# Kernel tuning notes

Measured on AMD Instinct MI355X. Metric: run time of the kernel, lower is better.

The kernel has to match this reference:

```python
import jax, jax.numpy as jnp
import numpy as np

D_MODEL = 1024
N_HEADS = 16
D_HEAD = D_MODEL // N_HEADS


def setup_inputs() -> dict:
    key = jax.random.key(0)
    ks = jax.random.split(key, 9)
    s = 1.0 / np.sqrt(D_MODEL)
    return {
        "x": jax.random.normal(ks[0], (4, 2048, D_MODEL), dtype=jnp.float32),
        "w_q": jax.random.uniform(ks[1], (D_MODEL, D_MODEL), jnp.float32, -s, s),
        "b_q": jax.random.uniform(ks[2], (D_MODEL,), jnp.float32, -s, s),
        "w_k": jax.random.uniform(ks[3], (D_MODEL, D_MODEL), jnp.float32, -s, s),
        "b_k": jax.random.uniform(ks[4], (D_MODEL,), jnp.float32, -s, s),
        "w_v": jax.random.uniform(ks[5], (D_MODEL, D_MODEL), jnp.float32, -s, s),
        "b_v": jax.random.uniform(ks[6], (D_MODEL,), jnp.float32, -s, s),
        "w_o": jax.random.uniform(ks[7], (D_MODEL, D_MODEL), jnp.float32, -s, s),
        "b_o": jax.random.uniform(ks[8], (D_MODEL,), jnp.float32, -s, s),
    }


def reference(x, w_q, b_q, w_k, b_k, w_v, b_v, w_o, b_o):
    B, S, _ = x.shape
    # Projections (torch Linear: x @ W.T + b), split into heads -> [B, H, S, Dh]
    def proj(w, b):
        return (x @ w.T + b).reshape(B, S, N_HEADS, D_HEAD).transpose(0, 2, 1, 3)

    q = proj(w_q, b_q)
    k = proj(w_k, b_k)
    v = proj(w_v, b_v)

    scale = 1.0 / np.sqrt(D_HEAD).astype(np.float32)
    scores = jnp.einsum("bhqd,bhkd->bhqk", q, k) * scale  # [B,H,S,S]
    attn = jax.nn.softmax(scores, axis=-1)  # dropout is identity in eval mode
    ctx = jnp.einsum("bhqk,bhkd->bhqd", attn, v)  # [B,H,S,Dh]
    ctx = ctx.transpose(0, 2, 1, 3).reshape(B, S, D_MODEL)
    return ctx @ w_o.T + b_o
```

## Files before the change

kernel.cpp:

```cpp
#include <hip/hip_runtime.h>
#include <hip/hip_bf16.h>

#define B_  4
#define S_  2048
#define D_  1024
#define H_  16
#define DH  64
#define M_  (B_ * S_)

typedef unsigned short u16;
typedef unsigned int u32;
typedef __attribute__((ext_vector_type(8))) short bf16x8;
typedef __attribute__((ext_vector_type(4))) float f32x4;
typedef __attribute__((ext_vector_type(4))) unsigned short u16x4;
typedef __attribute__((ext_vector_type(4))) unsigned int u32x4;

static __device__ __forceinline__ u16 f2bf(float x) {
    union { float f; unsigned u; } c;
    c.f = x;
    const unsigned u = c.u;
    return (u16)((u + 0x7FFFu + ((u >> 16) & 1u)) >> 16);
}
static __device__ __forceinline__ float bf2f(u16 h) {
    union { unsigned u; float f; } c;
    c.u = ((unsigned)h) << 16;
    return c.f;
}
#ifdef __BF16_MANT_DIG__
static __device__ __forceinline__ u16 f2bf_hw(float x) {
    __bf16 b = (__bf16)x;
    return __builtin_bit_cast(u16, b);
}
#else
#define f2bf_hw f2bf
#endif
#if __has_builtin(__builtin_amdgcn_exp2f)
#define fexp2 __builtin_amdgcn_exp2f
#else
#define fexp2 exp2f
#endif
static __device__ __forceinline__ void gl16(const u16* g, u16* l) {
    __builtin_amdgcn_global_load_lds(
        (const __attribute__((address_space(1))) unsigned int*)g,
        (__attribute__((address_space(3))) unsigned int*)l, 16, 0, 0);
}
static __device__ __forceinline__ u32 cvtpk(float a, float b) {
    u32 r;
    asm("v_cvt_pk_bf16_f32 %0, %1, %2" : "=v"(r) : "v"(a), "v"(b));
    return r;
}
static __device__ __forceinline__ void pswap32(u32& d, u32& s) {
    asm volatile("v_permlane32_swap_b32 %0, %1" : "+v"(d), "+v"(s));
}
static __device__ __forceinline__ void pswap16(u32& d, u32& s) {
    asm volatile("v_permlane16_swap_b32 %0, %1" : "+v"(d), "+v"(s));
}

__global__ __launch_bounds__(256) void prep(const float* __restrict__ x,
                                            const float* __restrict__ wq,
                                            const float* __restrict__ wk,
                                            const float* __restrict__ wv,
                                            const float* __restrict__ wo,
                                            u16* __restrict__ xh,
                                            u16* __restrict__ wh,
                                            u16* __restrict__ woh,
                                            u16* __restrict__ wol) {
    const size_t NX = (size_t)M_ * D_ / 4;
    const size_t NW = (size_t)D_ * D_ / 4;
    const size_t i = (size_t)blockIdx.x * 256 + threadIdx.x;
    if (i < NX) {
        float4 v = ((const float4*)x)[i];
        u16x4 h;
        h[0] = f2bf_hw(v.x); h[1] = f2bf_hw(v.y);
        h[2] = f2bf_hw(v.z); h[3] = f2bf_hw(v.w);
        ((u16x4*)xh)[i] = h;
    } else if (i < NX + 3 * NW) {
        const size_t j = i - NX;
        const int sel = (int)(j / NW);
        const size_t k = j - (size_t)sel * NW;
        const float* src = sel == 0 ? wq : sel == 1 ? wk : wv;
        float4 v = ((const float4*)src)[k];
        u16x4 h;
        h[0] = f2bf_hw(v.x); h[1] = f2bf_hw(v.y);
        h[2] = f2bf_hw(v.z); h[3] = f2bf_hw(v.w);
        ((u16x4*)(wh + (size_t)sel * D_ * D_))[k] = h;
    } else {
        const size_t k = i - NX - 3 * NW;
        float4 v = ((const float4*)wo)[k];
        u16x4 h, l;
        float vv[4] = {v.x, v.y, v.z, v.w};
#pragma unroll
        for (int j = 0; j < 4; ++j) {
            h[j] = f2bf_hw(vv[j]);
            l[j] = f2bf_hw(vv[j] - bf2f(h[j]));
        }
        ((u16x4*)woh)[k] = h;
        ((u16x4*)wol)[k] = l;
    }
}

__global__ __launch_bounds__(256) void gemm_qkv(const u16* __restrict__ xh,
                                                const u16* __restrict__ whb,
                                                const float* __restrict__ bq,
                                                const float* __restrict__ bk,
                                                const float* __restrict__ bv,
                                                u16* __restrict__ qb,
                                                u16* __restrict__ kb,
                                                u16* __restrict__ vt) {
    __shared__ __align__(16) u16 sA[8192];
    __shared__ __align__(16) u16 sB[8192];

    const int tid = threadIdx.x;
    const int l = tid & 63;
    const int w = tid >> 6;
    const int lo = l & 15;
    const int hi = l >> 4;
    const int wr = w >> 1;
    const int wc = w & 1;
    const int L = blockIdx.x;
    const int c = L & 7;
    const int t = L >> 3;
    const int by = c * 8 + (t & 7);
    const int bxs = t >> 3;
    const int wsel = bxs >> 3;
    const int bx = bxs & 7;
    const int m0 = by * 128;
    const int n0 = bx * 128;

    const u16* W = whb + (size_t)wsel * D_ * D_;
    const float* bias = wsel == 0 ? bq : wsel == 1 ? bk : bv;

    auto stage = [&](int k0, int half) {
#pragma unroll
        for (int i = 0; i < 2; ++i) {
            const int p = 256 * i + tid;
            const int row = p >> 2;
            const int ps = p & 3;
            const int sl = ps ^ ((row + (row >> 2)) & 3);
            const int lb = half * 4096 + (256 * i + 64 * w) * 8;
            gl16(xh + (size_t)(m0 + row) * D_ + k0 + 8 * sl, &sA[lb]);
            gl16(W + (size_t)(n0 + row) * D_ + k0 + 8 * sl, &sB[lb]);
        }
    };

    const f32x4 z4 = {0.f, 0.f, 0.f, 0.f};
    f32x4 acc[4][4];
#pragma unroll
    for (int i = 0; i < 4; ++i)
#pragma unroll
        for (int j = 0; j < 4; ++j) acc[i][j] = z4;

    stage(0, 0);
    for (int k0 = 0; k0 < D_; k0 += 32) {
        const int cur = (k0 >> 5) & 1;
        __syncthreads();
        if (k0 + 32 < D_) stage(k0 + 32, cur ^ 1);
        const int bufo = cur * 4096;

        bf16x8 ah[4], bh[4];
#pragma unroll
        for (int mi = 0; mi < 4; ++mi) {
            const int r = wr * 64 + mi * 16 + lo;
            const int sl = hi ^ ((r + (r >> 2)) & 3);
            ah[mi] = *(const bf16x8*)&sA[bufo + r * 32 + sl * 8];
        }
#pragma unroll
        for (int nj = 0; nj < 4; ++nj) {
            const int r = wc * 64 + nj * 16 + lo;
            const int sl = hi ^ ((r + (r >> 2)) & 3);
            bh[nj] = *(const bf16x8*)&sB[bufo + r * 32 + sl * 8];
        }
#pragma unroll
        for (int mi = 0; mi < 4; ++mi)
#pragma unroll
            for (int nj = 0; nj < 4; ++nj)
                acc[mi][nj] = __builtin_amdgcn_mfma_f32_16x16x32_bf16(
                    ah[mi], bh[nj], acc[mi][nj], 0, 0, 0);
    }

    float bv_[4];
#pragma unroll
    for (int nj = 0; nj < 4; ++nj) bv_[nj] = bias[n0 + wc * 64 + nj * 16 + lo];

#pragma unroll
    for (int mi = 0; mi < 4; ++mi)
#pragma unroll
        for (int nj = 0; nj < 4; ++nj)
#pragma unroll
            for (int r = 0; r < 4; ++r) {
                const float v = acc[mi][nj][r] + bv_[nj];
                const int cm = m0 + wr * 64 + mi * 16 + hi * 4 + r;
                const int cn = n0 + wc * 64 + nj * 16 + lo;
                const int b = cm >> 11, s = cm & (S_ - 1);
                const int h = cn >> 6, d = cn & 63;
                if (wsel == 0)
                    qb[(((size_t)b * H_ + h) * S_ + s) * DH + d] =
                        f2bf(v * 0.18033688011112042f);
                else if (wsel == 1)
                    kb[(((size_t)b * H_ + h) * S_ + s) * DH + d] = f2bf(v);
                else
                    vt[(((size_t)b * H_ + h) * DH + d) * S_ + s] = f2bf(v);
            }
}

__global__ __launch_bounds__(256) void gemm_out(const u16* __restrict__ Ah,
                                                const u16* __restrict__ Al,
                                                const u16* __restrict__ Wh,
                                                const u16* __restrict__ Wl,
                                                const float* __restrict__ bias,
                                                float* __restrict__ Cout) {
    __shared__ __align__(16) u16 sAh[8192];
    __shared__ __align__(16) u16 sBh[8192];
    __shared__ __align__(16) u16 sAl[8192];
    __shared__ __align__(16) u16 sBl[8192];

    const int tid = threadIdx.x;
    const int l = tid & 63;
    const int w = tid >> 6;
    const int lo = l & 15;
    const int hi = l >> 4;
    const int wr = w >> 1;
    const int wc = w & 1;
    const int L = blockIdx.x;
    const int c = L & 7;
    const int t = L >> 3;
    const int by = c * 8 + (t >> 3);
    const int bx = t & 7;
    const int m0 = by * 128;
    const int n0 = bx * 128;

    auto stage = [&](int k0, int half) {
#pragma unroll
        for (int i = 0; i < 2; ++i) {
            const int p = 256 * i + tid;
            const int row = p >> 2;
            const int ps = p & 3;
            const int sl = ps ^ ((row + (row >> 2)) & 3);
            const int lb = half * 4096 + (256 * i + 64 * w) * 8;
            const size_t ga = (size_t)(m0 + row) * D_ + k0 + 8 * sl;
            const size_t gb = (size_t)(n0 + row) * D_ + k0 + 8 * sl;
            gl16(Ah + ga, &sAh[lb]);
            gl16(Al + ga, &sAl[lb]);
            gl16(Wh + gb, &sBh[lb]);
            gl16(Wl + gb, &sBl[lb]);
        }
    };

    const f32x4 z4 = {0.f, 0.f, 0.f, 0.f};
    f32x4 acc[4][4];
#pragma unroll
    for (int i = 0; i < 4; ++i)
#pragma unroll
        for (int j = 0; j < 4; ++j) acc[i][j] = z4;

    stage(0, 0);
    for (int k0 = 0; k0 < D_; k0 += 32) {
        const int cur = (k0 >> 5) & 1;
        __syncthreads();
        if (k0 + 32 < D_) stage(k0 + 32, cur ^ 1);
        const int bufo = cur * 4096;

        bf16x8 ah[4], al_[4], bh[4], bl_[4];
#pragma unroll
        for (int mi = 0; mi < 4; ++mi) {
            const int r = wr * 64 + mi * 16 + lo;
            const int sl = hi ^ ((r + (r >> 2)) & 3);
            ah[mi] = *(const bf16x8*)&sAh[bufo + r * 32 + sl * 8];
            al_[mi] = *(const bf16x8*)&sAl[bufo + r * 32 + sl * 8];
        }
#pragma unroll
        for (int nj = 0; nj < 4; ++nj) {
            const int r = wc * 64 + nj * 16 + lo;
            const int sl = hi ^ ((r + (r >> 2)) & 3);
            bh[nj] = *(const bf16x8*)&sBh[bufo + r * 32 + sl * 8];
            bl_[nj] = *(const bf16x8*)&sBl[bufo + r * 32 + sl * 8];
        }
#pragma unroll
        for (int mi = 0; mi < 4; ++mi)
#pragma unroll
            for (int nj = 0; nj < 4; ++nj) {
                acc[mi][nj] = __builtin_amdgcn_mfma_f32_16x16x32_bf16(
                    ah[mi], bh[nj], acc[mi][nj], 0, 0, 0);
                acc[mi][nj] = __builtin_amdgcn_mfma_f32_16x16x32_bf16(
                    ah[mi], bl_[nj], acc[mi][nj], 0, 0, 0);
                acc[mi][nj] = __builtin_amdgcn_mfma_f32_16x16x32_bf16(
                    al_[mi], bh[nj], acc[mi][nj], 0, 0, 0);
            }
    }

    float bv_[4];
#pragma unroll
    for (int nj = 0; nj < 4; ++nj) bv_[nj] = bias[n0 + wc * 64 + nj * 16 + lo];

#pragma unroll
    for (int mi = 0; mi < 4; ++mi)
#pragma unroll
        for (int nj = 0; nj < 4; ++nj)
#pragma unroll
            for (int r = 0; r < 4; ++r) {
                const int cm = m0 + wr * 64 + mi * 16 + hi * 4 + r;
                const int cn = n0 + wc * 64 + nj * 16 + lo;
                Cout[(size_t)cm * D_ + cn] = acc[mi][nj][r] + bv_[nj];
            }
}

__global__ __launch_bounds__(256, 4) void attn6(const u16* __restrict__ Qb,
                                                const u16* __restrict__ Kb,
                                                const u16* __restrict__ Vtg,
                                                u16* __restrict__ chi,
                                                u16* __restrict__ clo) {
    __shared__ __align__(16) u16 KsA[2 * 4096];
    __shared__ __align__(16) u16 VsA[2 * 4096];

    const int tid = threadIdx.x;
    const int l = tid & 63;
    const int w = tid >> 6;
    const int lo = l & 15;
    const int hi = l >> 4;
    const int L = blockIdx.x;
    const int c = L & 7;
    const int t = L >> 3;
    const int bh = c * 8 + (t >> 4);
    const int s0 = (t & 15) * 128;
    const size_t base = (size_t)bh * S_ * DH;

    const int sp0 = tid;
    const int srow0 = sp0 >> 3, ssl0 = (sp0 & 7) ^ (srow0 & 7);
    const int sp1 = 256 + tid;
    const int srow1 = sp1 >> 3, ssl1 = (sp1 & 7) ^ (srow1 & 7);
    const int lb0 = (64 * w) * 8;
    const int lb1 = (256 + 64 * w) * 8;

    bf16x8 qa[2][2];
#pragma unroll
    for (int qh = 0; qh < 2; ++qh) {
        const u16* qp = Qb + base + (size_t)(s0 + w * 32 + qh * 16 + lo) * DH;
        qa[qh][0] = *(const bf16x8*)(qp + hi * 8);
        qa[qh][1] = *(const bf16x8*)(qp + hi * 8 + 32);
    }

    const f32x4 zero4 = {0.f, 0.f, 0.f, 0.f};
    f32x4 acc[2][4];
    f32x4 acc_l[2] = {zero4, zero4};
#pragma unroll
    for (int qh = 0; qh < 2; ++qh)
#pragma unroll
        for (int g = 0; g < 4; ++g) acc[qh][g] = zero4;

    const short onebf = (short)0x3F80;
    const bf16x8 ones = {onebf, onebf, onebf, onebf, onebf, onebf, onebf, onebf};

#define STAGE(KT, HALF)                                                        \
    do {                                                                       \
        const size_t kbase = base + (size_t)(KT) * 64 * DH;                    \
        const size_t vbase = base + (size_t)(KT) * 64;                         \
        gl16(Kb + kbase + (size_t)srow0 * DH + 8 * ssl0, &KsA[(HALF)*4096 + lb0]); \
        gl16(Vtg + vbase + (size_t)srow0 * S_ + 8 * ssl0, &VsA[(HALF)*4096 + lb0]); \
        gl16(Kb + kbase + (size_t)srow1 * DH + 8 * ssl1, &KsA[(HALF)*4096 + lb1]); \
        gl16(Vtg + vbase + (size_t)srow1 * S_ + 8 * ssl1, &VsA[(HALF)*4096 + lb1]); \
    } while (0)

    STAGE(0, 0);

    for (int kt = 0; kt < S_ / 64; ++kt) {
        const int cur = kt & 1;
        __syncthreads();
        if (kt + 1 < S_ / 64) STAGE(kt + 1, cur ^ 1);
        const u16* Ks = &KsA[cur * 4096];
        const u16* Vs = &VsA[cur * 4096];

        f32x4 sc[2][4];
#pragma unroll
        for (int qh = 0; qh < 2; ++qh)
#pragma unroll
            for (int f = 0; f < 4; ++f) sc[qh][f] = zero4;
        __builtin_amdgcn_s_setprio(1);
#pragma unroll
        for (int f = 0; f < 4; ++f) {
            const int kr = lo + 16 * f;
            const int ksw = (kr & 7) << 3;
#pragma unroll
            for (int ks = 0; ks < 2; ++ks) {
                bf16x8 kf = *(const bf16x8*)&Ks[kr * 64 + ((hi * 8 + 32 * ks) ^ ksw)];
                sc[0][f] = __builtin_amdgcn_mfma_f32_16x16x32_bf16(kf, qa[0][ks], sc[0][f], 0, 0, 0);
                sc[1][f] = __builtin_amdgcn_mfma_f32_16x16x32_bf16(kf, qa[1][ks], sc[1][f], 0, 0, 0);
            }
        }
        __builtin_amdgcn_s_setprio(0);

        bf16x8 pa[2][2];
#pragma unroll
        for (int qh = 0; qh < 2; ++qh) {
            u32 T[2][4];
#pragma unroll
            for (int ks = 0; ks < 2; ++ks)
#pragma unroll
                for (int cc = 0; cc < 2; ++cc) {
                    u32 X = cvtpk(fexp2(sc[qh][2 * ks][2 * cc]),
                                  fexp2(sc[qh][2 * ks][2 * cc + 1]));
                    u32 Y = cvtpk(fexp2(sc[qh][2 * ks + 1][2 * cc]),
                                  fexp2(sc[qh][2 * ks + 1][2 * cc + 1]));
                    pswap32(X, Y);
                    pswap16(X, Y);
                    T[ks][cc] = X;
                    T[ks][2 + cc] = Y;
                }
#pragma unroll
            for (int ks = 0; ks < 2; ++ks) {
                u32x4 word = {T[ks][0], T[ks][1], T[ks][2], T[ks][3]};
                pa[qh][ks] = __builtin_bit_cast(bf16x8, word);
            }
        }

        __builtin_amdgcn_s_setprio(1);
        acc_l[0] = __builtin_amdgcn_mfma_f32_16x16x32_bf16(ones, pa[0][0], acc_l[0], 0, 0, 0);
        acc_l[0] = __builtin_amdgcn_mfma_f32_16x16x32_bf16(ones, pa[0][1], acc_l[0], 0, 0, 0);
        acc_l[1] = __builtin_amdgcn_mfma_f32_16x16x32_bf16(ones, pa[1][0], acc_l[1], 0, 0, 0);
        acc_l[1] = __builtin_amdgcn_mfma_f32_16x16x32_bf16(ones, pa[1][1], acc_l[1], 0, 0, 0);
#pragma unroll
        for (int g = 0; g < 4; ++g) {
            const int vr = lo + 16 * g;
            const int vsw = (vr & 7) << 3;
#pragma unroll
            for (int ks = 0; ks < 2; ++ks) {
                bf16x8 vf = *(const bf16x8*)&Vs[vr * 64 + ((hi * 8 + 32 * ks) ^ vsw)];
                acc[0][g] = __builtin_amdgcn_mfma_f32_16x16x32_bf16(vf, pa[0][ks], acc[0][g], 0, 0, 0);
                acc[1][g] = __builtin_amdgcn_mfma_f32_16x16x32_bf16(vf, pa[1][ks], acc[1][g], 0, 0, 0);
            }
        }
        __builtin_amdgcn_s_setprio(0);
    }
#undef STAGE

    const int b = bh >> 4;
    const int h = bh & 15;
#pragma unroll
    for (int qh = 0; qh < 2; ++qh) {
        const float inv = 1.f / acc_l[qh][0];
        const int row = s0 + w * 32 + qh * 16 + lo;
#pragma unroll
        for (int g = 0; g < 4; ++g) {
            u16x4 hh, ll;
#pragma unroll
            for (int r = 0; r < 4; ++r) {
                const float v = acc[qh][g][r] * inv;
                hh[r] = f2bf_hw(v);
                ll[r] = f2bf_hw(v - bf2f(hh[r]));
            }
            const size_t off = ((size_t)b * S_ + row) * D_ + h * 64 + 16 * g + hi * 4;
            *(u16x4*)&chi[off] = hh;
            *(u16x4*)&clo[off] = ll;
        }
    }
}

extern "C" void kernel_launch(void* const* d_in, const int* in_sizes, int n_in,
                              void* d_out, int out_size, void* d_ws, size_t ws_size,
                              hipStream_t stream) {
    const float* x  = (const float*)d_in[0];
    const float* wq = (const float*)d_in[1];
    const float* bq = (const float*)d_in[2];
    const float* wk = (const float*)d_in[3];
    const float* bk = (const float*)d_in[4];
    const float* wv = (const float*)d_in[5];
    const float* bv = (const float*)d_in[6];
    const float* wo = (const float*)d_in[7];
    const float* bo = (const float*)d_in[8];
    float* out = (float*)d_out;

    const size_t MD = (size_t)M_ * D_;
    const size_t WD = (size_t)D_ * D_;
    u16* ws = (u16*)d_ws;
    u16* xh  = ws;
    u16* wh  = xh + MD;
    u16* woh = wh + 3 * WD;
    u16* wol = woh + WD;
    u16* qb  = wol + WD;
    u16* kb  = qb + MD;
    u16* vt  = kb + MD;
    u16* clo = vt + MD;
    u16* chi = xh;

    dim3 blk(256);
    prep<<<dim3(12288), blk, 0, stream>>>(x, wq, wk, wv, wo, xh, wh, woh, wol);
    gemm_qkv<<<dim3(1536), blk, 0, stream>>>(xh, wh, bq, bk, bv, qb, kb, vt);
    attn6<<<dim3(1024), blk, 0, stream>>>(qb, kb, vt, chi, clo);
    gemm_out<<<dim3(512), blk, 0, stream>>>(chi, clo, woh, wol, bo, out);
}
```

Baseline: 220.1 us.

## Triple-buffer LDS staging in projection GEMMs with partial vmcnt barriers

Both the QKV projection GEMM and the split-precision output GEMM move from double-buffered to triple-buffered LDS staging. Loads are issued two k-tiles ahead, and each iteration waits only on older loads using s_waitcnt vmcnt(4) plus s_barrier instead of __syncthreads. In the output GEMM the high-part tiles are triple-buffered and prefetched two ahead, while the low-part tiles stay double-buffered and are prefetched one ahead, which limits LDS growth. The goal is to hide global-load latency behind MFMA work, at the cost of more LDS per block, possibly lower occupancy, and a correctness dependence on the hand-counted vmcnt values.

```diff
diff --git a/kernel.cpp b/kernel.cpp
--- a/kernel.cpp
+++ b/kernel.cpp
@@ -55,6 +55,8 @@
 static __device__ __forceinline__ void pswap16(u32& d, u32& s) {
     asm volatile("v_permlane16_swap_b32 %0, %1" : "+v"(d), "+v"(s));
 }
+#define WAITBAR4() asm volatile("s_waitcnt vmcnt(4)\n\ts_barrier" ::: "memory")
+#define WAITBAR0() asm volatile("s_waitcnt vmcnt(0)\n\ts_barrier" ::: "memory")
 
 __global__ __launch_bounds__(256) void prep(const float* __restrict__ x,
                                             const float* __restrict__ wq,
@@ -107,8 +109,8 @@
                                                 u16* __restrict__ qb,
                                                 u16* __restrict__ kb,
                                                 u16* __restrict__ vt) {
-    __shared__ __align__(16) u16 sA[8192];
-    __shared__ __align__(16) u16 sB[8192];
+    __shared__ __align__(16) u16 sA[3 * 4096];
+    __shared__ __align__(16) u16 sB[3 * 4096];
 
     const int tid = threadIdx.x;
     const int l = tid & 63;
@@ -130,14 +132,14 @@
     const u16* W = whb + (size_t)wsel * D_ * D_;
     const float* bias = wsel == 0 ? bq : wsel == 1 ? bk : bv;
 
-    auto stage = [&](int k0, int half) {
+    auto stage = [&](int k0, int buf) {
 #pragma unroll
         for (int i = 0; i < 2; ++i) {
             const int p = 256 * i + tid;
             const int row = p >> 2;
             const int ps = p & 3;
             const int sl = ps ^ ((row + (row >> 2)) & 3);
-            const int lb = half * 4096 + (256 * i + 64 * w) * 8;
+            const int lb = buf * 4096 + (256 * i + 64 * w) * 8;
             gl16(xh + (size_t)(m0 + row) * D_ + k0 + 8 * sl, &sA[lb]);
             gl16(W + (size_t)(n0 + row) * D_ + k0 + 8 * sl, &sB[lb]);
         }
@@ -151,11 +153,12 @@
         for (int j = 0; j < 4; ++j) acc[i][j] = z4;
 
     stage(0, 0);
-    for (int k0 = 0; k0 < D_; k0 += 32) {
-        const int cur = (k0 >> 5) & 1;
-        __syncthreads();
-        if (k0 + 32 < D_) stage(k0 + 32, cur ^ 1);
-        const int bufo = cur * 4096;
+    stage(32, 1);
+    for (int kt = 0; kt < 32; ++kt) {
+        if (kt < 31) WAITBAR4();
+        else         WAITBAR0();
+        if (kt + 2 < 32) stage(32 * (kt + 2), (kt + 2) % 3);
+        const int bufo = (kt % 3) * 4096;
 
         bf16x8 ah[4], bh[4];
 #pragma unroll
@@ -209,10 +212,10 @@
                                                 const u16* __restrict__ Wl,
                                                 const float* __restrict__ bias,
                                                 float* __restrict__ Cout) {
-    __shared__ __align__(16) u16 sAh[8192];
-    __shared__ __align__(16) u16 sBh[8192];
-    __shared__ __align__(16) u16 sAl[8192];
-    __shared__ __align__(16) u16 sBl[8192];
+    __shared__ __align__(16) u16 sAh[3 * 4096];
+    __shared__ __align__(16) u16 sBh[3 * 4096];
+    __shared__ __align__(16) u16 sAl[2 * 4096];
+    __shared__ __align__(16) u16 sBl[2 * 4096];
 
     const int tid = threadIdx.x;
     const int l = tid & 63;
@@ -229,20 +232,28 @@
     const int m0 = by * 128;
     const int n0 = bx * 128;
 
-    auto stage = [&](int k0, int half) {
+    auto stage_hi = [&](int k0, int buf) {
 #pragma unroll
         for (int i = 0; i < 2; ++i) {
             const int p = 256 * i + tid;
             const int row = p >> 2;
             const int ps = p & 3;
             const int sl = ps ^ ((row + (row >> 2)) & 3);
-            const int lb = half * 4096 + (256 * i + 64 * w) * 8;
-            const size_t ga = (size_t)(m0 + row) * D_ + k0 + 8 * sl;
-            const size_t gb = (size_t)(n0 + row) * D_ + k0 + 8 * sl;
-            gl16(Ah + ga, &sAh[lb]);
-            gl16(Al + ga, &sAl[lb]);
-            gl16(Wh + gb, &sBh[lb]);
-            gl16(Wl + gb, &sBl[lb]);
+            const int lb = buf * 4096 + (256 * i + 64 * w) * 8;
+            gl16(Ah + (size_t)(m0 + row) * D_ + k0 + 8 * sl, &sAh[lb]);
+            gl16(Wh + (size_t)(n0 + row) * D_ + k0 + 8 * sl, &sBh[lb]);
+        }
+    };
+    auto stage_lo = [&](int k0, int buf) {
+#pragma unroll
+        for (int i = 0; i < 2; ++i) {
+            const int p = 256 * i + tid;
+            const int row = p >> 2;
+            const int ps = p & 3;
+            const int sl = ps ^ ((row + (row >> 2)) & 3);
+            const int lb = buf * 4096 + (256 * i + 64 * w) * 8;
+            gl16(Al + (size_t)(m0 + row) * D_ + k0 + 8 * sl, &sAl[lb]);
+            gl16(Wl + (size_t)(n0 + row) * D_ + k0 + 8 * sl, &sBl[lb]);
         }
     };
 
@@ -253,27 +264,31 @@
 #pragma unroll
         for (int j = 0; j < 4; ++j) acc[i][j] = z4;
 
-    stage(0, 0);
-    for (int k0 = 0; k0 < D_; k0 += 32) {
-        const int cur = (k0 >> 5) & 1;
-        __syncthreads();
-        if (k0 + 32 < D_) stage(k0 + 32, cur ^ 1);
-        const int bufo = cur * 4096;
+    stage_hi(0, 0);
+    stage_lo(0, 0);
+    stage_hi(32, 1);
+    for (int kt = 0; kt < 32; ++kt) {
+        if (kt < 31) WAITBAR4();
+        else         WAITBAR0();
+        if (kt + 1 < 32) stage_lo(32 * (kt + 1), (kt + 1) & 1);
+        if (kt + 2 < 32) stage_hi(32 * (kt + 2), (kt + 2) % 3);
+        const int bh_o = (kt % 3) * 4096;
+        const int bl_o = (kt & 1) * 4096;
 
         bf16x8 ah[4], al_[4], bh[4], bl_[4];
 #pragma unroll
         for (int mi = 0; mi < 4; ++mi) {
             const int r = wr * 64 + mi * 16 + lo;
             const int sl = hi ^ ((r + (r >> 2)) & 3);
-            ah[mi] = *(const bf16x8*)&sAh[bufo + r * 32 + sl * 8];
-            al_[mi] = *(const bf16x8*)&sAl[bufo + r * 32 + sl * 8];
+            ah[mi] = *(const bf16x8*)&sAh[bh_o + r * 32 + sl * 8];
+            al_[mi] = *(const bf16x8*)&sAl[bl_o + r * 32 + sl * 8];
         }
 #pragma unroll
         for (int nj = 0; nj < 4; ++nj) {
             const int r = wc * 64 + nj * 16 + lo;
             const int sl = hi ^ ((r + (r >> 2)) & 3);
-            bh[nj] = *(const bf16x8*)&sBh[bufo + r * 32 + sl * 8];
-            bl_[nj] = *(const bf16x8*)&sBl[bufo + r * 32 + sl * 8];
+            bh[nj] = *(const bf16x8*)&sBh[bh_o + r * 32 + sl * 8];
+            bl_[nj] = *(const bf16x8*)&sBl[bl_o + r * 32 + sl * 8];
         }
 #pragma unroll
         for (int mi = 0; mi < 4; ++mi)
```

New measurement: 238.0 us. 8.1% more time.
